# Kernel optimization log

Measured on AMD Instinct MI355X. Metric: run time of the kernel, lower is better.

## Reference

```python
import jax, jax.numpy as jnp
import numpy as np

N = 100000      # nodes
E = 1600000     # edges
D_IN = 100
D_OUT = 100


def _sage(x, src, dst, W_agg, W_root, b):
    """PyG SAGEConv, aggr='mean', root_weight=True:
    out = mean_{j in N(i)} x_j @ W_agg + x_i @ W_root + b
    Aggregation flows source -> target (dst gathers from src)."""
    num_nodes = x.shape[0]
    deg = jax.ops.segment_sum(jnp.ones((src.shape[0],), x.dtype), dst,
                              num_segments=num_nodes)
    agg = jax.ops.segment_sum(x[src], dst, num_segments=num_nodes)  # [N, D]
    agg = agg / jnp.maximum(deg, 1.0)[:, None]
    return agg @ W_agg + x @ W_root + b


def setup_inputs() -> dict:
    key = jax.random.key(0)
    ks = jax.random.split(key, 12)
    s = 0.05
    return {
        "x": jax.random.normal(ks[0], (N, D_IN), jnp.float32),
        "edge_index": jax.random.randint(ks[1], (2, E), 0, N, jnp.int32),
        "edge_weight": jax.random.uniform(ks[2], (E,), jnp.float32),
        "W_sage_agg": jax.random.normal(ks[3], (D_IN, D_OUT), jnp.float32) * s,
        "W_sage_root": jax.random.normal(ks[4], (D_IN, D_OUT), jnp.float32) * s,
        "b_sage": jnp.zeros((D_OUT,), jnp.float32),
        "W_mu_agg": jax.random.normal(ks[5], (D_OUT, D_OUT), jnp.float32) * s,
        "W_mu_root": jax.random.normal(ks[6], (D_OUT, D_OUT), jnp.float32) * s,
        "b_mu": jnp.zeros((D_OUT,), jnp.float32),
        "W_var_agg": jax.random.normal(ks[7], (D_OUT, D_OUT), jnp.float32) * s,
        "W_var_root": jax.random.normal(ks[8], (D_OUT, D_OUT), jnp.float32) * s,
        "b_var": jnp.zeros((D_OUT,), jnp.float32),
    }


def reference(x, edge_index, edge_weight,
              W_sage_agg, W_sage_root, b_sage,
              W_mu_agg, W_mu_root, b_mu,
              W_var_agg, W_var_root, b_var):
    # edge_weight is accepted but unused, matching the torch module.
    src, dst = edge_index[0], edge_index[1]
    feat = jax.nn.relu(_sage(x, src, dst, W_sage_agg, W_sage_root, b_sage))
    mu = _sage(feat, src, dst, W_mu_agg, W_mu_root, b_mu)
    var = _sage(feat, src, dst, W_var_agg, W_var_root, b_var)
    return (mu, var)
```

## Files before the change

### kernel.cpp

```cpp
#include <hip/hip_runtime.h>
#include <cstdint>
#include <cstddef>

#define N_NODES 100000
#define N_EDGES 1600000
#define DIM 100
#define DPAD 128
#define ROWS_ALLOC 100096

#define KBUCK 500
#define NPB   200
#define BCAP  4096
#define EPB   6400

typedef __attribute__((ext_vector_type(8))) short s16x8;
typedef __attribute__((ext_vector_type(8))) unsigned short us8;
typedef __attribute__((ext_vector_type(4))) float f32x4;

static __device__ __forceinline__ float bf2f(unsigned short h) {
    return __uint_as_float(((unsigned)h) << 16);
}
static __device__ __forceinline__ unsigned short f2bf(float f) {
    unsigned u = __float_as_uint(f);
    return (unsigned short)((u + 0x7FFFu + ((u >> 16) & 1u)) >> 16);
}

__global__ __launch_bounds__(256) void bucket_kernel(const int* __restrict__ ei,
                                                     unsigned* __restrict__ bucket_cur,
                                                     unsigned* __restrict__ regions) {
    __shared__ unsigned hist[KBUCK];
    __shared__ unsigned posl[KBUCK];
    int tid = threadIdx.x;
    int e0 = blockIdx.x * EPB;
    for (int i = tid; i < KBUCK; i += 256) hist[i] = 0;
    __syncthreads();
    for (int i = tid; i < EPB; i += 256) {
        int dst = ei[N_EDGES + e0 + i];
        int b = dst / NPB;
        atomicAdd(&hist[b], 1u);
    }
    __syncthreads();
    for (int i = tid; i < KBUCK; i += 256) {
        unsigned h = hist[i];
        posl[i] = h ? atomicAdd(&bucket_cur[i], h) : 0u;
    }
    __syncthreads();
    for (int i = tid; i < EPB; i += 256) {
        int src = ei[e0 + i];
        int dst = ei[N_EDGES + e0 + i];
        int b = dst / NPB;
        int dl = dst - b * NPB;
        unsigned r = atomicAdd(&posl[b], 1u);
        if (r < BCAP) regions[(size_t)b * BCAP + r] = ((unsigned)src << 8) | (unsigned)dl;
    }
}

__global__ __launch_bounds__(256) void csr_kernel(const unsigned* __restrict__ regions,
                                                  const unsigned* __restrict__ bucket_cur,
                                                  unsigned* __restrict__ gbase,
                                                  int* __restrict__ row_off,
                                                  int* __restrict__ cnt,
                                                  int* __restrict__ csr_src) {
    __shared__ unsigned hist[256];
    __shared__ unsigned sa[256], sb[256];
    __shared__ unsigned posl[256];
    __shared__ unsigned sh_gb;
    int tid = threadIdx.x;
    int b = blockIdx.x;
    unsigned total = bucket_cur[b];
    if (total > BCAP) total = BCAP;
    hist[tid] = 0;
    __syncthreads();
    const unsigned* reg = regions + (size_t)b * BCAP;
    for (unsigned e = tid; e < total; e += 256)
        atomicAdd(&hist[reg[e] & 0xFFu], 1u);
    __syncthreads();
    unsigned* cur = sa; unsigned* nxt = sb;
    cur[tid] = hist[tid];
    __syncthreads();
    for (int off = 1; off < 256; off <<= 1) {
        unsigned t = cur[tid];
        if (tid >= off) t += cur[tid - off];
        nxt[tid] = t;
        __syncthreads();
        unsigned* tmp = cur; cur = nxt; nxt = tmp;
    }
    unsigned excl = cur[tid] - hist[tid];
    if (tid == 0) sh_gb = atomicAdd(gbase, total);
    __syncthreads();
    unsigned gb = sh_gb;
    posl[tid] = gb + excl;
    if (tid < NPB) {
        int node = b * NPB + tid;
        cnt[node] = (int)hist[tid];
        row_off[node] = (int)(gb + excl);
    }
    __syncthreads();
    for (unsigned e = tid; e < total; e += 256) {
        unsigned p = reg[e];
        unsigned r = atomicAdd(&posl[p & 0xFFu], 1u);
        csr_src[r] = (int)(p >> 8);
    }
}

__global__ __launch_bounds__(256) void convert_pad(const float* __restrict__ X,
                                                   unsigned short* __restrict__ Xp) {
    int t = blockIdx.x * 256 + threadIdx.x;
    if (t >= N_NODES * 16) return;
    int node = t >> 4, chunk = t & 15;
    us8 o;
    if (chunk < 12) {
        const float4* p = (const float4*)(X + (size_t)node * DIM + chunk * 8);
        float4 a = p[0], b = p[1];
        o[0] = f2bf(a.x); o[1] = f2bf(a.y); o[2] = f2bf(a.z); o[3] = f2bf(a.w);
        o[4] = f2bf(b.x); o[5] = f2bf(b.y); o[6] = f2bf(b.z); o[7] = f2bf(b.w);
    } else if (chunk == 12) {
        const float4* p = (const float4*)(X + (size_t)node * DIM + 96);
        float4 a = p[0];
        o[0] = f2bf(a.x); o[1] = f2bf(a.y); o[2] = f2bf(a.z); o[3] = f2bf(a.w);
        o[4] = 0; o[5] = 0; o[6] = 0; o[7] = 0;
    } else {
        for (int i = 0; i < 8; ++i) o[i] = 0;
    }
    *(us8*)(Xp + (size_t)node * DPAD + chunk * 8) = o;
}

__global__ __launch_bounds__(256) void build_w(const float* __restrict__ W0, const float* __restrict__ W1,
                                               const float* __restrict__ W2, const float* __restrict__ W3,
                                               const float* __restrict__ W4, const float* __restrict__ W5,
                                               unsigned short* __restrict__ Wt) {
    int t = blockIdx.x * 256 + threadIdx.x;
    if (t >= 6 * DPAD * 16) return;
    int mat = t / (DPAD * 16);
    int rem = t % (DPAD * 16);
    int nrow = rem >> 4, chunk = rem & 15;
    const float* W = (mat == 0) ? W0 : (mat == 1) ? W1 : (mat == 2) ? W2
                   : (mat == 3) ? W3 : (mat == 4) ? W4 : W5;
    us8 o;
    #pragma unroll
    for (int j = 0; j < 8; ++j) {
        int k = chunk * 8 + j;
        float v = (k < DIM && nrow < DIM) ? W[(size_t)k * DIM + nrow] : 0.f;
        o[j] = f2bf(v);
    }
    *(us8*)(Wt + (size_t)mat * DPAD * DPAD + (size_t)nrow * DPAD + chunk * 8) = o;
}

__global__ __launch_bounds__(256) void build_bias(const float* __restrict__ b0, const float* __restrict__ b1,
                                                  const float* __restrict__ b2, float* __restrict__ bp) {
    int t = blockIdx.x * 256 + threadIdx.x;
    if (t >= 3 * DPAD) return;
    int mat = t / DPAD, i = t % DPAD;
    const float* b = (mat == 0) ? b0 : (mat == 1) ? b1 : b2;
    bp[t] = (i < DIM) ? b[i] : 0.f;
}

__global__ __launch_bounds__(256) void aggregate_pad(const unsigned short* __restrict__ Xh,
                                                     const int* __restrict__ csr_src,
                                                     const int* __restrict__ row_off,
                                                     const int* __restrict__ cnt,
                                                     unsigned short* __restrict__ outh, int n) {
    int node = blockIdx.x * 4 + (threadIdx.x >> 6);
    if (node >= n) return;
    int lane = threadIdx.x & 63;
    int chunk = lane & 15;
    int slot  = lane >> 4;
    int start = row_off[node];
    int deg   = cnt[node];
    float acc[8];
    #pragma unroll
    for (int i = 0; i < 8; ++i) acc[i] = 0.f;
    for (int base = 0; base < deg; base += 64) {
        int m = deg - base; if (m > 64) m = 64;
        int sv = (lane < m) ? csr_src[start + base + lane] : 0;
        #pragma unroll 4
        for (int j = 0; j < m; j += 4) {
            int s = __shfl(sv, j + slot, 64);
            if (j + slot < m) {
                us8 u = *(const us8*)(Xh + (size_t)s * DPAD + chunk * 8);
                #pragma unroll
                for (int i = 0; i < 8; ++i) acc[i] += bf2f(u[i]);
            }
        }
    }
    #pragma unroll
    for (int i = 0; i < 8; ++i) {
        acc[i] += __shfl_xor(acc[i], 16, 64);
        acc[i] += __shfl_xor(acc[i], 32, 64);
    }
    if (lane < 16) {
        float inv = 1.0f / (float)(deg > 0 ? deg : 1);
        us8 o;
        #pragma unroll
        for (int i = 0; i < 8; ++i) o[i] = f2bf(acc[i] * inv);
        *(us8*)(outh + (size_t)node * DPAD + chunk * 8) = o;
    }
}

__global__ __launch_bounds__(256) void gemm_l1_mfma(const unsigned short* __restrict__ Aagg,
                                                    const unsigned short* __restrict__ Aroot,
                                                    const unsigned short* __restrict__ WtA,
                                                    const unsigned short* __restrict__ WtR,
                                                    const float* __restrict__ bpad,
                                                    unsigned short* __restrict__ outp, int nrows) {
    int lane = threadIdx.x & 63;
    int wv   = threadIdx.x >> 6;
    int m16  = lane & 15;
    int quad = lane >> 4;
    int wrow = blockIdx.x * 128 + wv * 32;

    f32x4 acc[2][8];
    #pragma unroll
    for (int rt = 0; rt < 2; ++rt)
        #pragma unroll
        for (int nt = 0; nt < 8; ++nt)
            acc[rt][nt] = (f32x4){0.f, 0.f, 0.f, 0.f};

    const unsigned short* As[2] = {Aagg, Aroot};
    const unsigned short* Ws[2] = {WtA, WtR};
    #pragma unroll
    for (int ph = 0; ph < 2; ++ph) {
        const unsigned short* A  = As[ph];
        const unsigned short* Wt = Ws[ph];
        s16x8 af[2][4];
        #pragma unroll
        for (int rt = 0; rt < 2; ++rt)
            #pragma unroll
            for (int ks = 0; ks < 4; ++ks)
                af[rt][ks] = *(const s16x8*)(A + (size_t)(wrow + rt * 16 + m16) * DPAD + ks * 32 + quad * 8);
        #pragma unroll
        for (int nt = 0; nt < 8; ++nt) {
            #pragma unroll
            for (int ks = 0; ks < 4; ++ks) {
                s16x8 bf = *(const s16x8*)(Wt + (size_t)(nt * 16 + m16) * DPAD + ks * 32 + quad * 8);
                acc[0][nt] = __builtin_amdgcn_mfma_f32_16x16x32_bf16(af[0][ks], bf, acc[0][nt], 0, 0, 0);
                acc[1][nt] = __builtin_amdgcn_mfma_f32_16x16x32_bf16(af[1][ks], bf, acc[1][nt], 0, 0, 0);
            }
        }
    }

    #pragma unroll
    for (int nt = 0; nt < 8; ++nt) {
        int col = nt * 16 + m16;
        float bias = bpad[col];
        #pragma unroll
        for (int rt = 0; rt < 2; ++rt) {
            #pragma unroll
            for (int reg = 0; reg < 4; ++reg) {
                int row = wrow + rt * 16 + quad * 4 + reg;
                if (row < nrows) {
                    float v = acc[rt][nt][reg] + bias;
                    v = v > 0.f ? v : 0.f;
                    outp[(size_t)row * DPAD + col] = f2bf(v);
                }
            }
        }
    }
}

__global__ __launch_bounds__(256) void gemm_l2_mfma(const unsigned short* __restrict__ Aagg,
                                                    const unsigned short* __restrict__ Afeat,
                                                    const unsigned short* __restrict__ WtMA,
                                                    const unsigned short* __restrict__ WtMR,
                                                    const unsigned short* __restrict__ WtVA,
                                                    const unsigned short* __restrict__ WtVR,
                                                    const float* __restrict__ bpm,
                                                    const float* __restrict__ bpv,
                                                    float* __restrict__ outMu,
                                                    float* __restrict__ outVar, int nrows) {
    int lane = threadIdx.x & 63;
    int wv   = threadIdx.x >> 6;
    int m16  = lane & 15;
    int quad = lane >> 4;
    int wrow = blockIdx.x * 128 + wv * 32;

    f32x4 accM[2][8], accV[2][8];
    #pragma unroll
    for (int rt = 0; rt < 2; ++rt)
        #pragma unroll
        for (int nt = 0; nt < 8; ++nt) {
            accM[rt][nt] = (f32x4){0.f, 0.f, 0.f, 0.f};
            accV[rt][nt] = (f32x4){0.f, 0.f, 0.f, 0.f};
        }

    const unsigned short* As[2]  = {Aagg, Afeat};
    const unsigned short* WsM[2] = {WtMA, WtMR};
    const unsigned short* WsV[2] = {WtVA, WtVR};
    #pragma unroll
    for (int ph = 0; ph < 2; ++ph) {
        const unsigned short* A   = As[ph];
        const unsigned short* WtM = WsM[ph];
        const unsigned short* WtV = WsV[ph];
        s16x8 af[2][4];
        #pragma unroll
        for (int rt = 0; rt < 2; ++rt)
            #pragma unroll
            for (int ks = 0; ks < 4; ++ks)
                af[rt][ks] = *(const s16x8*)(A + (size_t)(wrow + rt * 16 + m16) * DPAD + ks * 32 + quad * 8);
        #pragma unroll
        for (int nt = 0; nt < 8; ++nt) {
            #pragma unroll
            for (int ks = 0; ks < 4; ++ks) {
                size_t boff = (size_t)(nt * 16 + m16) * DPAD + ks * 32 + quad * 8;
                s16x8 bm = *(const s16x8*)(WtM + boff);
                s16x8 bv = *(const s16x8*)(WtV + boff);
                accM[0][nt] = __builtin_amdgcn_mfma_f32_16x16x32_bf16(af[0][ks], bm, accM[0][nt], 0, 0, 0);
                accM[1][nt] = __builtin_amdgcn_mfma_f32_16x16x32_bf16(af[1][ks], bm, accM[1][nt], 0, 0, 0);
                accV[0][nt] = __builtin_amdgcn_mfma_f32_16x16x32_bf16(af[0][ks], bv, accV[0][nt], 0, 0, 0);
                accV[1][nt] = __builtin_amdgcn_mfma_f32_16x16x32_bf16(af[1][ks], bv, accV[1][nt], 0, 0, 0);
            }
        }
    }

    #pragma unroll
    for (int nt = 0; nt < 8; ++nt) {
        int col = nt * 16 + m16;
        if (col >= DIM) continue;
        float bm = bpm[col], bv = bpv[col];
        #pragma unroll
        for (int rt = 0; rt < 2; ++rt) {
            #pragma unroll
            for (int reg = 0; reg < 4; ++reg) {
                int row = wrow + rt * 16 + quad * 4 + reg;
                if (row < nrows) {
                    outMu [(size_t)row * DIM + col] = accM[rt][nt][reg] + bm;
                    outVar[(size_t)row * DIM + col] = accV[rt][nt][reg] + bv;
                }
            }
        }
    }
}

extern "C" void kernel_launch(void* const* d_in, const int* in_sizes, int n_in,
                              void* d_out, int out_size, void* d_ws, size_t ws_size,
                              hipStream_t stream) {
    const float* x   = (const float*)d_in[0];
    const int*   ei  = (const int*)d_in[1];
    const float* Wsa = (const float*)d_in[3];
    const float* Wsr = (const float*)d_in[4];
    const float* bs  = (const float*)d_in[5];
    const float* Wma = (const float*)d_in[6];
    const float* Wmr = (const float*)d_in[7];
    const float* bm  = (const float*)d_in[8];
    const float* Wva = (const float*)d_in[9];
    const float* Wvr = (const float*)d_in[10];
    const float* bv  = (const float*)d_in[11];

    float* out_mu  = (float*)d_out;
    float* out_var = out_mu + (size_t)N_NODES * DIM;

    char* ws = (char*)d_ws;
    int*      row_off    = (int*)(ws);
    int*      cnt        = (int*)(ws + 400000);
    unsigned* bucket_cur = (unsigned*)(ws + 800000);
    unsigned* gbase      = (unsigned*)(ws + 802048);
    int*      csr_src    = (int*)(ws + 802176);
    unsigned short* Wt   = (unsigned short*)(ws + 7202176);
    float*          bp   = (float*)(ws + 7398784);
    unsigned short* xp   = (unsigned short*)(ws + 7400448);
    unsigned short* aggp = (unsigned short*)(ws + 33025024);
    unsigned short* ftp  = (unsigned short*)(ws + 58649600);
    unsigned* regions    = (unsigned*)(ws + 7400448);

    unsigned short* WtSA = Wt;
    unsigned short* WtSR = Wt + 1 * DPAD * DPAD;
    unsigned short* WtMA = Wt + 2 * DPAD * DPAD;
    unsigned short* WtMR = Wt + 3 * DPAD * DPAD;
    unsigned short* WtVA = Wt + 4 * DPAD * DPAD;
    unsigned short* WtVR = Wt + 5 * DPAD * DPAD;
    float* bps = bp;
    float* bpm = bp + DPAD;
    float* bpv = bp + 2 * DPAD;

    hipMemsetAsync(bucket_cur, 0, 2048, stream);
    hipMemsetAsync(gbase, 0, 128, stream);

    bucket_kernel<<<N_EDGES / EPB, 256, 0, stream>>>(ei, bucket_cur, regions);
    csr_kernel<<<KBUCK, 256, 0, stream>>>(regions, bucket_cur, gbase, row_off, cnt, csr_src);

    convert_pad<<<(N_NODES * 16 + 255) / 256, 256, 0, stream>>>(x, xp);
    build_w<<<(6 * DPAD * 16 + 255) / 256, 256, 0, stream>>>(Wsa, Wsr, Wma, Wmr, Wva, Wvr, Wt);
    build_bias<<<2, 256, 0, stream>>>(bs, bm, bv, bp);

    aggregate_pad<<<N_NODES / 4, 256, 0, stream>>>(xp, csr_src, row_off, cnt, aggp, N_NODES);
    gemm_l1_mfma<<<ROWS_ALLOC / 128, 256, 0, stream>>>(aggp, xp, WtSA, WtSR, bps, ftp, N_NODES);

    aggregate_pad<<<N_NODES / 4, 256, 0, stream>>>(ftp, csr_src, row_off, cnt, aggp, N_NODES);
    gemm_l2_mfma<<<ROWS_ALLOC / 128, 256, 0, stream>>>(aggp, ftp, WtMA, WtMR, WtVA, WtVR,
                                                       bpm, bpv, out_mu, out_var, N_NODES);
}
```

Measured before the change: 466.8 us.

## Restructure dense GEMMs so each wave holds a weight column strip in registers

Both layer GEMM kernels now assign each wave a fixed 32-column output strip and keep that strip's weight fragments in registers. Each block walks 64 rows, with the weight as MFMA A operand and activations as B, so the accumulator layout gives contiguous 4-column outputs. Stores become vectorized (us4 for bf16 features, float4 for fp32 outputs), replacing scattered scalar writes and repeated weight reloads per row tile. The trade-off is that each activation row is now read by all four waves of a block, relying on cache hits.

```diff
diff --git a/kernel.cpp b/kernel.cpp
--- a/kernel.cpp
+++ b/kernel.cpp
@@ -15,6 +15,7 @@
 
 typedef __attribute__((ext_vector_type(8))) short s16x8;
 typedef __attribute__((ext_vector_type(8))) unsigned short us8;
+typedef __attribute__((ext_vector_type(4))) unsigned short us4;
 typedef __attribute__((ext_vector_type(4))) float f32x4;
 
 static __device__ __forceinline__ float bf2f(unsigned short h) {
@@ -197,134 +198,137 @@
     }
 }
 
-__global__ __launch_bounds__(256) void gemm_l1_mfma(const unsigned short* __restrict__ Aagg,
-                                                    const unsigned short* __restrict__ Aroot,
-                                                    const unsigned short* __restrict__ WtA,
-                                                    const unsigned short* __restrict__ WtR,
-                                                    const float* __restrict__ bpad,
-                                                    unsigned short* __restrict__ outp, int nrows) {
-    int lane = threadIdx.x & 63;
-    int wv   = threadIdx.x >> 6;
-    int m16  = lane & 15;
-    int quad = lane >> 4;
-    int wrow = blockIdx.x * 128 + wv * 32;
-
-    f32x4 acc[2][8];
-    #pragma unroll
-    for (int rt = 0; rt < 2; ++rt)
-        #pragma unroll
-        for (int nt = 0; nt < 8; ++nt)
-            acc[rt][nt] = (f32x4){0.f, 0.f, 0.f, 0.f};
-
-    const unsigned short* As[2] = {Aagg, Aroot};
+__global__ __launch_bounds__(256) void gemm_l1_strip(const unsigned short* __restrict__ Aagg,
+                                                     const unsigned short* __restrict__ Aroot,
+                                                     const unsigned short* __restrict__ WtA,
+                                                     const unsigned short* __restrict__ WtR,
+                                                     const float* __restrict__ bpad,
+                                                     unsigned short* __restrict__ outp) {
+    int lane  = threadIdx.x & 63;
+    int strip = threadIdx.x >> 6;
+    int m16   = lane & 15;
+    int quad  = lane >> 4;
+    int row0  = blockIdx.x * 64;
+
+    s16x8 wf[2][2][4];
     const unsigned short* Ws[2] = {WtA, WtR};
     #pragma unroll
-    for (int ph = 0; ph < 2; ++ph) {
-        const unsigned short* A  = As[ph];
-        const unsigned short* Wt = Ws[ph];
-        s16x8 af[2][4];
-        #pragma unroll
-        for (int rt = 0; rt < 2; ++rt)
+    for (int ph = 0; ph < 2; ++ph)
+        #pragma unroll
+        for (int nt = 0; nt < 2; ++nt)
             #pragma unroll
             for (int ks = 0; ks < 4; ++ks)
-                af[rt][ks] = *(const s16x8*)(A + (size_t)(wrow + rt * 16 + m16) * DPAD + ks * 32 + quad * 8);
-        #pragma unroll
-        for (int nt = 0; nt < 8; ++nt) {
+                wf[ph][nt][ks] = *(const s16x8*)(Ws[ph] + (size_t)(strip * 32 + nt * 16 + m16) * DPAD + ks * 32 + quad * 8);
+
+    float4 bias4[2];
+    #pragma unroll
+    for (int nt = 0; nt < 2; ++nt)
+        bias4[nt] = *(const float4*)(bpad + strip * 32 + nt * 16 + quad * 4);
+
+    #pragma unroll
+    for (int t = 0; t < 4; ++t) {
+        int m = row0 + t * 16 + m16;
+        s16x8 afA[4], afR[4];
+        #pragma unroll
+        for (int ks = 0; ks < 4; ++ks) {
+            afA[ks] = *(const s16x8*)(Aagg  + (size_t)m * DPAD + ks * 32 + quad * 8);
+            afR[ks] = *(const s16x8*)(Aroot + (size_t)m * DPAD + ks * 32 + quad * 8);
+        }
+        f32x4 acc[2];
+        acc[0] = (f32x4){0.f, 0.f, 0.f, 0.f};
+        acc[1] = (f32x4){0.f, 0.f, 0.f, 0.f};
+        #pragma unroll
+        for (int ks = 0; ks < 4; ++ks) {
+            acc[0] = __builtin_amdgcn_mfma_f32_16x16x32_bf16(wf[0][0][ks], afA[ks], acc[0], 0, 0, 0);
+            acc[1] = __builtin_amdgcn_mfma_f32_16x16x32_bf16(wf[0][1][ks], afA[ks], acc[1], 0, 0, 0);
+            acc[0] = __builtin_amdgcn_mfma_f32_16x16x32_bf16(wf[1][0][ks], afR[ks], acc[0], 0, 0, 0);
+            acc[1] = __builtin_amdgcn_mfma_f32_16x16x32_bf16(wf[1][1][ks], afR[ks], acc[1], 0, 0, 0);
+        }
+        #pragma unroll
+        for (int nt = 0; nt < 2; ++nt) {
+            int col0 = strip * 32 + nt * 16 + quad * 4;
+            us4 o;
             #pragma unroll
-            for (int ks = 0; ks < 4; ++ks) {
-                s16x8 bf = *(const s16x8*)(Wt + (size_t)(nt * 16 + m16) * DPAD + ks * 32 + quad * 8);
-                acc[0][nt] = __builtin_amdgcn_mfma_f32_16x16x32_bf16(af[0][ks], bf, acc[0][nt], 0, 0, 0);
-                acc[1][nt] = __builtin_amdgcn_mfma_f32_16x16x32_bf16(af[1][ks], bf, acc[1][nt], 0, 0, 0);
+            for (int r = 0; r < 4; ++r) {
+                float v = acc[nt][r] + ((const float*)&bias4[nt])[r];
+                v = v > 0.f ? v : 0.f;
+                o[r] = f2bf(v);
             }
-        }
-    }
-
-    #pragma unroll
-    for (int nt = 0; nt < 8; ++nt) {
-        int col = nt * 16 + m16;
-        float bias = bpad[col];
-        #pragma unroll
-        for (int rt = 0; rt < 2; ++rt) {
+            *(us4*)(outp + (size_t)m * DPAD + col0) = o;
+        }
+    }
+}
+
+__global__ __launch_bounds__(256) void gemm_l2_strip(const unsigned short* __restrict__ Aagg,
+                                                     const unsigned short* __restrict__ Afeat,
+                                                     const unsigned short* __restrict__ WtMA,
+                                                     const unsigned short* __restrict__ WtMR,
+                                                     const unsigned short* __restrict__ WtVA,
+                                                     const unsigned short* __restrict__ WtVR,
+                                                     const float* __restrict__ bpm,
+                                                     const float* __restrict__ bpv,
+                                                     float* __restrict__ outMu,
+                                                     float* __restrict__ outVar) {
+    int lane  = threadIdx.x & 63;
+    int strip = threadIdx.x >> 6;
+    int m16   = lane & 15;
+    int quad  = lane >> 4;
+    int row0  = blockIdx.x * 64;
+
+    s16x8 wf[2][2][2][4];
+    const unsigned short* Ws[2][2] = {{WtMA, WtMR}, {WtVA, WtVR}};
+    #pragma unroll
+    for (int hd = 0; hd < 2; ++hd)
+        #pragma unroll
+        for (int ph = 0; ph < 2; ++ph)
             #pragma unroll
-            for (int reg = 0; reg < 4; ++reg) {
-                int row = wrow + rt * 16 + quad * 4 + reg;
-                if (row < nrows) {
-                    float v = acc[rt][nt][reg] + bias;
-                    v = v > 0.f ? v : 0.f;
-                    outp[(size_t)row * DPAD + col] = f2bf(v);
-                }
-            }
-        }
-    }
-}
-
-__global__ __launch_bounds__(256) void gemm_l2_mfma(const unsigned short* __restrict__ Aagg,
-                                                    const unsigned short* __restrict__ Afeat,
-                                                    const unsigned short* __restrict__ WtMA,
-                                                    const unsigned short* __restrict__ WtMR,
-                                                    const unsigned short* __restrict__ WtVA,
-                                                    const unsigned short* __restrict__ WtVR,
-                                                    const float* __restrict__ bpm,
-                                                    const float* __restrict__ bpv,
-                                                    float* __restrict__ outMu,
-                                                    float* __restrict__ outVar, int nrows) {
-    int lane = threadIdx.x & 63;
-    int wv   = threadIdx.x >> 6;
-    int m16  = lane & 15;
-    int quad = lane >> 4;
-    int wrow = blockIdx.x * 128 + wv * 32;
-
-    f32x4 accM[2][8], accV[2][8];
-    #pragma unroll
-    for (int rt = 0; rt < 2; ++rt)
-        #pragma unroll
-        for (int nt = 0; nt < 8; ++nt) {
-            accM[rt][nt] = (f32x4){0.f, 0.f, 0.f, 0.f};
-            accV[rt][nt] = (f32x4){0.f, 0.f, 0.f, 0.f};
-        }
-
-    const unsigned short* As[2]  = {Aagg, Afeat};
-    const unsigned short* WsM[2] = {WtMA, WtMR};
-    const unsigned short* WsV[2] = {WtVA, WtVR};
-    #pragma unroll
-    for (int ph = 0; ph < 2; ++ph) {
-        const unsigned short* A   = As[ph];
-        const unsigned short* WtM = WsM[ph];
-        const unsigned short* WtV = WsV[ph];
-        s16x8 af[2][4];
-        #pragma unroll
-        for (int rt = 0; rt < 2; ++rt)
+            for (int nt = 0; nt < 2; ++nt)
+                #pragma unroll
+                for (int ks = 0; ks < 4; ++ks)
+                    wf[hd][ph][nt][ks] = *(const s16x8*)(Ws[hd][ph] + (size_t)(strip * 32 + nt * 16 + m16) * DPAD + ks * 32 + quad * 8);
+
+    float4 bm4[2], bv4[2];
+    #pragma unroll
+    for (int nt = 0; nt < 2; ++nt) {
+        bm4[nt] = *(const float4*)(bpm + strip * 32 + nt * 16 + quad * 4);
+        bv4[nt] = *(const float4*)(bpv + strip * 32 + nt * 16 + quad * 4);
+    }
+
+    #pragma unroll
+    for (int t = 0; t < 4; ++t) {
+        int m = row0 + t * 16 + m16;
+        s16x8 afA[4], afF[4];
+        #pragma unroll
+        for (int ks = 0; ks < 4; ++ks) {
+            afA[ks] = *(const s16x8*)(Aagg  + (size_t)m * DPAD + ks * 32 + quad * 8);
+            afF[ks] = *(const s16x8*)(Afeat + (size_t)m * DPAD + ks * 32 + quad * 8);
+        }
+        f32x4 aM[2], aV[2];
+        aM[0] = (f32x4){0.f,0.f,0.f,0.f}; aM[1] = (f32x4){0.f,0.f,0.f,0.f};
+        aV[0] = (f32x4){0.f,0.f,0.f,0.f}; aV[1] = (f32x4){0.f,0.f,0.f,0.f};
+        #pragma unroll
+        for (int ks = 0; ks < 4; ++ks) {
+            aM[0] = __builtin_amdgcn_mfma_f32_16x16x32_bf16(wf[0][0][0][ks], afA[ks], aM[0], 0, 0, 0);
+            aM[1] = __builtin_amdgcn_mfma_f32_16x16x32_bf16(wf[0][0][1][ks], afA[ks], aM[1], 0, 0, 0);
+            aV[0] = __builtin_amdgcn_mfma_f32_16x16x32_bf16(wf[1][0][0][ks], afA[ks], aV[0], 0, 0, 0);
+            aV[1] = __builtin_amdgcn_mfma_f32_16x16x32_bf16(wf[1][0][1][ks], afA[ks], aV[1], 0, 0, 0);
+            aM[0] = __builtin_amdgcn_mfma_f32_16x16x32_bf16(wf[0][1][0][ks], afF[ks], aM[0], 0, 0, 0);
+            aM[1] = __builtin_amdgcn_mfma_f32_16x16x32_bf16(wf[0][1][1][ks], afF[ks], aM[1], 0, 0, 0);
+            aV[0] = __builtin_amdgcn_mfma_f32_16x16x32_bf16(wf[1][1][0][ks], afF[ks], aV[0], 0, 0, 0);
+            aV[1] = __builtin_amdgcn_mfma_f32_16x16x32_bf16(wf[1][1][1][ks], afF[ks], aV[1], 0, 0, 0);
+        }
+        if (m < N_NODES) {
             #pragma unroll
-            for (int ks = 0; ks < 4; ++ks)
-                af[rt][ks] = *(const s16x8*)(A + (size_t)(wrow + rt * 16 + m16) * DPAD + ks * 32 + quad * 8);
-        #pragma unroll
-        for (int nt = 0; nt < 8; ++nt) {
-            #pragma unroll
-            for (int ks = 0; ks < 4; ++ks) {
-                size_t boff = (size_t)(nt * 16 + m16) * DPAD + ks * 32 + quad * 8;
-                s16x8 bm = *(const s16x8*)(WtM + boff);
-                s16x8 bv = *(const s16x8*)(WtV + boff);
-                accM[0][nt] = __builtin_amdgcn_mfma_f32_16x16x32_bf16(af[0][ks], bm, accM[0][nt], 0, 0, 0);
-                accM[1][nt] = __builtin_amdgcn_mfma_f32_16x16x32_bf16(af[1][ks], bm, accM[1][nt], 0, 0, 0);
-                accV[0][nt] = __builtin_amdgcn_mfma_f32_16x16x32_bf16(af[0][ks], bv, accV[0][nt], 0, 0, 0);
-                accV[1][nt] = __builtin_amdgcn_mfma_f32_16x16x32_bf16(af[1][ks], bv, accV[1][nt], 0, 0, 0);
-            }
-        }
-    }
-
-    #pragma unroll
-    for (int nt = 0; nt < 8; ++nt) {
-        int col = nt * 16 + m16;
-        if (col >= DIM) continue;
-        float bm = bpm[col], bv = bpv[col];
-        #pragma unroll
-        for (int rt = 0; rt < 2; ++rt) {
-            #pragma unroll
-            for (int reg = 0; reg < 4; ++reg) {
-                int row = wrow + rt * 16 + quad * 4 + reg;
-                if (row < nrows) {
-                    outMu [(size_t)row * DIM + col] = accM[rt][nt][reg] + bm;
-                    outVar[(size_t)row * DIM + col] = accV[rt][nt][reg] + bv;
+            for (int nt = 0; nt < 2; ++nt) {
+                int col0 = strip * 32 + nt * 16 + quad * 4;
+                if (col0 <= DIM - 4) {
+                    float4 vm, vv;
+                    vm.x = aM[nt][0] + bm4[nt].x; vm.y = aM[nt][1] + bm4[nt].y;
+                    vm.z = aM[nt][2] + bm4[nt].z; vm.w = aM[nt][3] + bm4[nt].w;
+                    vv.x = aV[nt][0] + bv4[nt].x; vv.y = aV[nt][1] + bv4[nt].y;
+                    vv.z = aV[nt][2] + bv4[nt].z; vv.w = aV[nt][3] + bv4[nt].w;
+                    *(float4*)(outMu  + (size_t)m * DIM + col0) = vm;
+                    *(float4*)(outVar + (size_t)m * DIM + col0) = vv;
                 }
             }
         }
@@ -383,9 +387,9 @@
     build_bias<<<2, 256, 0, stream>>>(bs, bm, bv, bp);
 
     aggregate_pad<<<N_NODES / 4, 256, 0, stream>>>(xp, csr_src, row_off, cnt, aggp, N_NODES);
-    gemm_l1_mfma<<<ROWS_ALLOC / 128, 256, 0, stream>>>(aggp, xp, WtSA, WtSR, bps, ftp, N_NODES);
+    gemm_l1_strip<<<ROWS_ALLOC / 64, 256, 0, stream>>>(aggp, xp, WtSA, WtSR, bps, ftp);
 
     aggregate_pad<<<N_NODES / 4, 256, 0, stream>>>(ftp, csr_src, row_off, cnt, aggp, N_NODES);
-    gemm_l2_mfma<<<ROWS_ALLOC / 128, 256, 0, stream>>>(aggp, ftp, WtMA, WtMR, WtVA, WtVR,
-                                                       bpm, bpv, out_mu, out_var, N_NODES);
-}
+    gemm_l2_strip<<<ROWS_ALLOC / 64, 256, 0, stream>>>(aggp, ftp, WtMA, WtMR, WtVA, WtVR,
+                                                       bpm, bpv, out_mu, out_var);
+}
```

New measurement: 418.4 us. 1.12x faster.
